# Performance work log

Hardware: AMD Instinct MI355X
Metric: run time of the kernel (lower is better)

## Reference

```python
import jax, jax.numpy as jnp
import numpy as np

DIM = 384
EPS = 1e-12  # F.normalize default eps


def setup_inputs() -> dict:
    key = jax.random.key(0)
    ks = jax.random.split(key, 6)
    b, c, h, w = 4, DIM, 64, 64
    x = jax.random.normal(ks[0], (b, c, h, w), dtype=jnp.float32)
    gamma = jnp.ones((c,), dtype=jnp.float32)  # WanRMS_norm gamma, init ones
    # 1x1 convs are per-pixel linear maps: [out_c, in_c] weight + bias
    w_qkv = jax.random.normal(ks[1], (3 * c, c), dtype=jnp.float32) * (1.0 / np.sqrt(c))
    b_qkv = jax.random.normal(ks[2], (3 * c,), dtype=jnp.float32) * 0.01
    w_proj = jax.random.normal(ks[3], (c, c), dtype=jnp.float32) * (1.0 / np.sqrt(c))
    b_proj = jax.random.normal(ks[4], (c,), dtype=jnp.float32) * 0.01
    return {"x": x, "gamma": gamma, "w_qkv": w_qkv, "b_qkv": b_qkv,
            "w_proj": w_proj, "b_proj": b_proj}


def reference(x, gamma, w_qkv, b_qkv, w_proj, b_proj):
    b, c, h, w = x.shape
    identity = x
    # WanRMS_norm: F.normalize over channel dim * sqrt(dim) * gamma
    l2 = jnp.sqrt(jnp.sum(x * x, axis=1, keepdims=True))
    xn = x / jnp.maximum(l2, EPS) * jnp.sqrt(jnp.float32(c)) * gamma[None, :, None, None]
    # 1x1 conv qkv: [b, 3c, h, w]
    qkv = jnp.einsum("bchw,oc->bohw", xn, w_qkv) + b_qkv[None, :, None, None]
    # flatten spatial -> tokens: [b, 3c, s] -> q/k/v each [b, s, c]
    s = h * w
    qkv = qkv.reshape(b, 3 * c, s).transpose(0, 2, 1)  # [b, s, 3c]
    q, k, v = jnp.split(qkv, 3, axis=-1)
    # single-head scaled dot-product attention (non-causal, as in Wan SDPA call)
    scores = jnp.einsum("bqc,bkc->bqk", q, k) / jnp.sqrt(jnp.float32(c))
    attn = jax.nn.softmax(scores, axis=-1)
    out = jnp.einsum("bqk,bkc->bqc", attn, v)  # [b, s, c]
    out = out.transpose(0, 2, 1).reshape(b, c, h, w)
    # 1x1 proj conv + residual
    out = jnp.einsum("bchw,oc->bohw", out, w_proj) + b_proj[None, :, None, None]
    return out + identity
```

## Files before the change

kernel.cpp:

```cpp
#include <hip/hip_runtime.h>
#include <cstdint>
#include <cstddef>

typedef __bf16 bf16;
typedef __bf16 bf16x8 __attribute__((ext_vector_type(8)));
typedef float  f32x4 __attribute__((ext_vector_type(4)));
typedef float  f32x16 __attribute__((ext_vector_type(16)));
typedef int    i32x4 __attribute__((ext_vector_type(4)));
typedef int    i32x8 __attribute__((ext_vector_type(8)));

#define MFMA16(a, b, c) __builtin_amdgcn_mfma_f32_16x16x32_bf16((a), (b), (c), 0, 0, 0)
#define MFMA_MX(a, b, c) \
    __builtin_amdgcn_mfma_scale_f32_32x32x64_f8f6f4((a), (b), (c), 0, 0, 0, 0x7F, 0, 0x7F)

#if __has_builtin(__builtin_amdgcn_exp2f)
#define EXP2(x) __builtin_amdgcn_exp2f(x)
#else
#define EXP2(x) exp2f(x)
#endif

__device__ __forceinline__ uint8_t to_fp8(float v) {
    return (uint8_t)(__builtin_amdgcn_cvt_pk_fp8_f32(v, v, 0, false) & 0xff);
}

__device__ __forceinline__ i32x8 ld32(const void* p) {
    i32x4 a = *(const i32x4*)p;
    i32x4 b = *(const i32x4*)((const char*)p + 16);
    i32x8 r;
    r[0] = a[0]; r[1] = a[1]; r[2] = a[2]; r[3] = a[3];
    r[4] = b[0]; r[5] = b[1]; r[6] = b[2]; r[7] = b[3];
    return r;
}

__device__ __forceinline__ void gload16(const void* g, void* l) {
    __builtin_amdgcn_global_load_lds(
        (const __attribute__((address_space(1))) unsigned int*)g,
        (__attribute__((address_space(3))) unsigned int*)l,
        16, 0, 0);
}

__global__ __launch_bounds__(256) void norm_kernel(
    const float* __restrict__ x, const float* __restrict__ gamma,
    const float* __restrict__ wqkv, const float* __restrict__ wproj,
    bf16* __restrict__ xn, bf16* __restrict__ wq, bf16* __restrict__ wp)
{
    const int tid = threadIdx.x;
    const int blk = blockIdx.x;
    if (blk >= 256) {
        int t0 = (blk - 256) * 256 + tid;
        for (int t = t0; t < 1152 * 384 + 384 * 384; t += 128 * 256) {
            if (t < 1152 * 384) wq[t] = (bf16)wqkv[t];
            else                wp[t - 1152 * 384] = (bf16)wproj[t - 1152 * 384];
        }
        return;
    }
    __shared__ float sG[384];
    __shared__ float sS[4][64];
    __shared__ float sScale[64];
    __shared__ bf16  sT[64][392];
    const int w = tid >> 6, l = tid & 63;
    for (int i = tid; i < 384; i += 256) sG[i] = gamma[i];
    const int b = blk >> 6, p0 = (blk & 63) << 6;
    const float* xc = x + ((size_t)(b * 384 + 96 * w)) * 4096 + p0 + l;
    float v[96];
    float s0 = 0.f, s1 = 0.f;
#pragma unroll
    for (int c = 0; c < 96; c += 2) {
        v[c]     = xc[(size_t)c * 4096];
        v[c + 1] = xc[(size_t)(c + 1) * 4096];
        s0 += v[c] * v[c]; s1 += v[c + 1] * v[c + 1];
    }
    sS[w][l] = s0 + s1;
    __syncthreads();
    if (w == 0) {
        float t = (sS[0][l] + sS[1][l]) + (sS[2][l] + sS[3][l]);
        sScale[l] = 19.595917942265423f / fmaxf(sqrtf(t), 1e-12f);
    }
    __syncthreads();
    float sc = sScale[l];
#pragma unroll
    for (int c0 = 0; c0 < 96; c0 += 8) {
        bf16x8 v8;
#pragma unroll
        for (int j = 0; j < 8; ++j)
            v8[j] = (bf16)(v[c0 + j] * sc * sG[96 * w + c0 + j]);
        *(bf16x8*)(&sT[l][96 * w + c0]) = v8;
    }
    __syncthreads();
    const int r = tid >> 2, seg = tid & 3;
    const bf16* srow = &sT[r][seg * 96];
    bf16* drow = xn + (size_t)((b << 12) + p0 + r) * 384 + seg * 96;
#pragma unroll
    for (int j = 0; j < 12; ++j)
        *(i32x4*)(drow + j * 8) = *(const i32x4*)(srow + j * 8);
}

__device__ __forceinline__ void gemm_core_bt(
    bf16* sA, bf16* sB,
    const bf16* __restrict__ A, const bf16* __restrict__ B,
    const float* __restrict__ bias_m, const float* __restrict__ bias_n,
    uint8_t* __restrict__ Cout, const int mode, const int ldc,
    const int m0, const int n0)
{
    const int tid = threadIdx.x;
    const int l = tid & 63, w = tid >> 6;
    const int lo = l & 15, hi = l >> 4;
    const int wm = w >> 1, wn = w & 1;

    f32x4 acc[4][4] = {};

    for (int kt = 0; kt < 6; ++kt) {
        __syncthreads();
        const int k0 = kt * 64;
#pragma unroll
        for (int i = 0; i < 5; ++i) {
            int ci = i * 256 + tid;
            if (ci < 1152) {
                int row = ci / 9, off = ci % 9;
                gload16(A + (size_t)(m0 + row) * 384 + k0 + off * 8, (char*)sA + ci * 16);
                gload16(B + (size_t)(n0 + row) * 384 + k0 + off * 8, (char*)sB + ci * 16);
            }
        }
        __syncthreads();
#pragma unroll
        for (int ks = 0; ks < 2; ++ks) {
            bf16x8 af[4], bfr[4];
#pragma unroll
            for (int t = 0; t < 4; ++t)
                af[t] = *(const bf16x8*)(sA + (wm * 64 + t * 16 + lo) * 72 + ks * 32 + hi * 8);
#pragma unroll
            for (int t = 0; t < 4; ++t)
                bfr[t] = *(const bf16x8*)(sB + (wn * 64 + t * 16 + lo) * 72 + ks * 32 + hi * 8);
#pragma unroll
            for (int rt = 0; rt < 4; ++rt)
#pragma unroll
                for (int ct = 0; ct < 4; ++ct)
                    acc[rt][ct] = MFMA16(af[rt], bfr[ct], acc[rt][ct]);
        }
    }

#pragma unroll
    for (int rt = 0; rt < 4; ++rt) {
#pragma unroll
        for (int ct = 0; ct < 4; ++ct) {
            int mb = m0 + wm * 64 + rt * 16 + hi * 4;
            int n  = n0 + wn * 64 + ct * 16 + lo;
            if (mode == 0) {
                float bn = bias_n[n];
#pragma unroll
                for (int r = 0; r < 4; ++r)
                    Cout[(size_t)(mb + r) * ldc + n] = to_fp8(acc[rt][ct][r] + bn);
            } else {
#pragma unroll
                for (int r = 0; r < 4; ++r)
                    Cout[(size_t)(mb + r) * ldc + n] = to_fp8(acc[rt][ct][r] + bias_m[mb + r]);
            }
        }
    }
}

__global__ __launch_bounds__(256) void gemm_qkv(
    const bf16* __restrict__ xn, const bf16* __restrict__ wq,
    const float* __restrict__ b_qkv, uint8_t* __restrict__ qkb,
    uint8_t* __restrict__ vtb)
{
    __shared__ bf16 sA[128 * 72];
    __shared__ bf16 sB[128 * 72];
    const int id = blockIdx.x;
    if (id < 768) {
        const int xcd = id & 7, s = id >> 3;
        gemm_core_bt(sA, sB, xn, wq, nullptr, b_qkv, qkb, 0, 768,
                     (xcd * 16 + s / 6) * 128, (s % 6) * 128);
    } else {
        const int t = id - 768;
        const int xcd = t & 7, s = t >> 3;
        gemm_core_bt(sA, sB, wq + (size_t)768 * 384, xn, b_qkv + 768, nullptr,
                     vtb, 1, 16384, (s % 3) * 128, (xcd * 16 + s / 3) * 128);
    }
}

__global__ __launch_bounds__(256) void gemm_proj(
    const bf16* __restrict__ wp, const bf16* __restrict__ p0,
    const bf16* __restrict__ p1, const float* __restrict__ ml,
    const float* __restrict__ b_proj, const float* __restrict__ x,
    float* __restrict__ out)
{
    __shared__ bf16 sA[128 * 72];
    __shared__ bf16 sB[128 * 72];
    const int tid = threadIdx.x;
    const int l = tid & 63, w = tid >> 6;
    const int lo = l & 15, hi = l >> 4;
    const int wm = w >> 1, wn = w & 1;
    const int id = blockIdx.x;
    const int xcd = id & 7, s = id >> 3;
    const int m0 = (s % 3) * 128, n0 = (xcd * 16 + s / 3) * 128;

    f32x4 acc[4][4] = {};

    for (int kt = 0; kt < 6; ++kt) {
        __syncthreads();
        const int k0 = kt * 64;
#pragma unroll
        for (int i = 0; i < 5; ++i) {
            int ci = i * 256 + tid;
            if (ci < 1152) {
                int row = ci / 9, off = ci % 9;
                gload16(wp + (size_t)(m0 + row) * 384 + k0 + off * 8, (char*)sA + ci * 16);
                int tok = n0 + row;
                float2 ml0 = *(const float2*)(ml + (size_t)tok * 2);
                float2 ml1 = *(const float2*)(ml + (size_t)(16384 + tok) * 2);
                float mM = fmaxf(ml0.x, ml1.x);
                float a0 = EXP2(ml0.x - mM), a1 = EXP2(ml1.x - mM);
                float inv = 1.0f / (a0 * ml0.y + a1 * ml1.y);
                float w0 = a0 * inv, w1 = a1 * inv;
                size_t boff = (size_t)tok * 384 + k0 + off * 8;
                bf16x8 v0 = *(const bf16x8*)(p0 + boff);
                bf16x8 v1 = *(const bf16x8*)(p1 + boff);
                bf16x8 r;
#pragma unroll
                for (int j = 0; j < 8; ++j)
                    r[j] = (bf16)((float)v0[j] * w0 + (float)v1[j] * w1);
                *(bf16x8*)((char*)sB + ci * 16) = r;
            }
        }
        __syncthreads();
#pragma unroll
        for (int ks = 0; ks < 2; ++ks) {
            bf16x8 af[4], bfr[4];
#pragma unroll
            for (int t = 0; t < 4; ++t)
                af[t] = *(const bf16x8*)(sA + (wm * 64 + t * 16 + lo) * 72 + ks * 32 + hi * 8);
#pragma unroll
            for (int t = 0; t < 4; ++t)
                bfr[t] = *(const bf16x8*)(sB + (wn * 64 + t * 16 + lo) * 72 + ks * 32 + hi * 8);
#pragma unroll
            for (int rt = 0; rt < 4; ++rt)
#pragma unroll
                for (int ct = 0; ct < 4; ++ct)
                    acc[rt][ct] = MFMA16(af[rt], bfr[ct], acc[rt][ct]);
        }
    }

#pragma unroll
    for (int rt = 0; rt < 4; ++rt) {
#pragma unroll
        for (int ct = 0; ct < 4; ++ct) {
            int mb = m0 + wm * 64 + rt * 16 + hi * 4;
            int n  = n0 + wn * 64 + ct * 16 + lo;
            int bb = n >> 12, p = n & 4095;
#pragma unroll
            for (int r = 0; r < 4; ++r) {
                int m = mb + r;
                size_t idx = ((size_t)(bb * 384 + m)) * 4096 + p;
                out[idx] = acc[rt][ct][r] + b_proj[m] + x[idx];
            }
        }
    }
}

__global__ __launch_bounds__(256, 2) void flash_kernel(
    const uint8_t* __restrict__ qk, const uint8_t* __restrict__ vt,
    bf16* __restrict__ op0, bf16* __restrict__ op1, float* __restrict__ ml)
{
    extern __shared__ char smem[];
    uint8_t* sbase = (uint8_t*)smem;
    uint8_t* sV = sbase + 51200;
    const int tid = threadIdx.x;
    const int l = tid & 63, w = tid >> 6;
    const int l31 = l & 31, hi2 = l >> 5;
    const int wq = w >> 1, wd = w & 1;
    const int id = blockIdx.x;
    const int qt = id >> 3, bh = id & 7;
    const int b = bh >> 1, half = bh & 1;
    const int q0 = b * 4096 + (qt & 63) * 64;
    const int kvbase = b * 4096 + half * 2048;
    const int rev = (id >> 8) & 1;
    const int kvstart = kvbase + (rev ? 31 * 64 : 0);
    const int kstep = rev ? -49152 : 49152;
    const int vstep = rev ? -64 : 64;
    const float SC = 0.07362217057594547f;
    const float THR = 108.664f;

    uint32_t ksrc[7];
#pragma unroll
    for (int i = 0; i < 7; ++i) {
        int ci = i * 256 + tid;
        int row = ci / 25, off = ci % 25;
        ksrc[i] = (uint32_t)((kvstart + row) * 768 + 384 + off * 16);
    }
    uint32_t vsrc[8];
#pragma unroll
    for (int i = 0; i < 8; ++i) {
        int ci = i * 256 + tid;
        int row = ci / 5, off = ci % 5;
        vsrc[i] = (uint32_t)(row * 16384 + kvstart + off * 16);
    }
#pragma unroll
    for (int i = 0; i < 7; ++i) {
        if (i < 6 || tid < 64) gload16(qk + ksrc[i], sbase + i * 4096 + tid * 16);
        ksrc[i] += (uint32_t)kstep;
    }

    i32x8 qf[6];
    {
        const uint8_t* qrow = qk + (size_t)(q0 + wq * 32 + l31) * 768 + hi2 * 32;
#pragma unroll
        for (int ksw = 0; ksw < 6; ++ksw)
            qf[ksw] = ld32(qrow + ksw * 64);
    }

    f32x16 o[6] = {};
    float m = -1e30f, lsum = 0.f;

    __syncthreads();

    int c = 0;
    for (int kt = 0; kt < 32; ++kt) {
#pragma unroll
        for (int i = 0; i < 8; ++i) {
            if (i < 7 || tid < 128) gload16(vt + vsrc[i], sV + i * 4096 + tid * 16);
            vsrc[i] += (uint32_t)vstep;
        }
        if (kt < 31) {
            uint8_t* dst = sbase + (c ^ 1) * 25600;
#pragma unroll
            for (int i = 0; i < 7; ++i) {
                if (i < 6 || tid < 64) gload16(qk + ksrc[i], dst + i * 4096 + tid * 16);
                ksrc[i] += (uint32_t)kstep;
            }
        }

        const uint8_t* sK = sbase + c * 25600;
        f32x16 s0 = {}, s1 = {};
        __builtin_amdgcn_s_setprio(1);
#pragma unroll
        for (int ksw = 0; ksw < 6; ++ksw) {
            i32x8 ak0 = ld32(sK + (size_t)l31 * 400 + ksw * 64 + hi2 * 32);
            i32x8 ak1 = ld32(sK + (size_t)(32 + l31) * 400 + ksw * 64 + hi2 * 32);
            s0 = MFMA_MX(ak0, qf[ksw], s0);
            s1 = MFMA_MX(ak1, qf[ksw], s1);
        }
        __builtin_amdgcn_s_setprio(0);

        float a0 = fmaxf(fmaxf(s0[0],  s0[1]),  fmaxf(s0[2],  s0[3]));
        float a1 = fmaxf(fmaxf(s0[4],  s0[5]),  fmaxf(s0[6],  s0[7]));
        float a2 = fmaxf(fmaxf(s0[8],  s0[9]),  fmaxf(s0[10], s0[11]));
        float a3 = fmaxf(fmaxf(s0[12], s0[13]), fmaxf(s0[14], s0[15]));
        float b0 = fmaxf(fmaxf(s1[0],  s1[1]),  fmaxf(s1[2],  s1[3]));
        float b1 = fmaxf(fmaxf(s1[4],  s1[5]),  fmaxf(s1[6],  s1[7]));
        float b2 = fmaxf(fmaxf(s1[8],  s1[9]),  fmaxf(s1[10], s1[11]));
        float b3 = fmaxf(fmaxf(s1[12], s1[13]), fmaxf(s1[14], s1[15]));
        float mx = fmaxf(fmaxf(fmaxf(a0, a1), fmaxf(a2, a3)),
                         fmaxf(fmaxf(b0, b1), fmaxf(b2, b3)));
        mx = fmaxf(mx, __shfl_xor(mx, 32));
        if (__any(mx > m + THR)) {
            float mn = fmaxf(m, mx);
            float alpha = EXP2((m - mn) * SC);
            m = mn;
            lsum *= alpha;
#pragma unroll
            for (int dt = 0; dt < 6; ++dt)
#pragma unroll
                for (int r = 0; r < 16; ++r) o[dt][r] *= alpha;
        }
        float p0[16], p1[16];
        float msc = m * SC;
        float rsa = 0.f, rsb = 0.f, rsc = 0.f, rsd = 0.f;
#pragma unroll
        for (int r = 0; r < 16; r += 4) {
            p0[r]     = EXP2(fmaf(s0[r],     SC, -msc)); rsa += p0[r];
            p0[r + 1] = EXP2(fmaf(s0[r + 1], SC, -msc)); rsb += p0[r + 1];
            p0[r + 2] = EXP2(fmaf(s0[r + 2], SC, -msc)); rsc += p0[r + 2];
            p0[r + 3] = EXP2(fmaf(s0[r + 3], SC, -msc)); rsd += p0[r + 3];
        }
#pragma unroll
        for (int r = 0; r < 16; r += 4) {
            p1[r]     = EXP2(fmaf(s1[r],     SC, -msc)); rsa += p1[r];
            p1[r + 1] = EXP2(fmaf(s1[r + 1], SC, -msc)); rsb += p1[r + 1];
            p1[r + 2] = EXP2(fmaf(s1[r + 2], SC, -msc)); rsc += p1[r + 2];
            p1[r + 3] = EXP2(fmaf(s1[r + 3], SC, -msc)); rsd += p1[r + 3];
        }
        float rs = (rsa + rsb) + (rsc + rsd);
        rs += __shfl_xor(rs, 32);
        lsum += rs;

        int pk0[4], pk1[4];
#pragma unroll
        for (int i = 0; i < 4; ++i) {
            int d = __builtin_amdgcn_cvt_pk_fp8_f32(p0[4 * i], p0[4 * i + 1], 0, false);
            pk0[i] = __builtin_amdgcn_cvt_pk_fp8_f32(p0[4 * i + 2], p0[4 * i + 3], d, true);
            d = __builtin_amdgcn_cvt_pk_fp8_f32(p1[4 * i], p1[4 * i + 1], 0, false);
            pk1[i] = __builtin_amdgcn_cvt_pk_fp8_f32(p1[4 * i + 2], p1[4 * i + 3], d, true);
        }
        i32x8 pf;
#pragma unroll
        for (int i = 0; i < 4; ++i) {
            int x0 = __shfl_xor(pk0[i], 32);
            int x1 = __shfl_xor(pk1[i], 32);
            int own = hi2 ? pk1[i] : pk0[i];
            int oth = hi2 ? x1 : x0;
            pf[2 * i]     = hi2 ? oth : own;
            pf[2 * i + 1] = hi2 ? own : oth;
        }

        __syncthreads();

        __builtin_amdgcn_s_setprio(1);
#pragma unroll
        for (int dt = 0; dt < 6; ++dt) {
            i32x8 av = ld32(sV + (size_t)(wd * 192 + dt * 32 + l31) * 80 + hi2 * 32);
            o[dt] = MFMA_MX(av, pf, o[dt]);
        }
        __builtin_amdgcn_s_setprio(0);

        __syncthreads();
        c ^= 1;
    }

    float* tr = (float*)(smem + w * 4608);
    bf16* dst = half ? op1 : op0;
#pragma unroll
    for (int dt = 0; dt < 6; ++dt) {
#pragma unroll
        for (int r = 0; r < 16; ++r) {
            int d32 = (r & 3) + 8 * (r >> 2) + 4 * hi2;
            tr[l31 * 36 + d32] = o[dt][r];
        }
        f32x4 v0 = *(f32x4*)(tr + l31 * 36 + hi2 * 16 + 0);
        f32x4 v1 = *(f32x4*)(tr + l31 * 36 + hi2 * 16 + 4);
        f32x4 v2 = *(f32x4*)(tr + l31 * 36 + hi2 * 16 + 8);
        f32x4 v3 = *(f32x4*)(tr + l31 * 36 + hi2 * 16 + 12);
        bf16x8 h0, h1;
#pragma unroll
        for (int j = 0; j < 4; ++j) {
            h0[j] = (bf16)v0[j]; h0[4 + j] = (bf16)v1[j];
            h1[j] = (bf16)v2[j]; h1[4 + j] = (bf16)v3[j];
        }
        size_t tok = (size_t)(q0 + wq * 32 + l31);
        bf16* drow = dst + tok * 384 + wd * 192 + dt * 32 + hi2 * 16;
        *(bf16x8*)(drow + 0) = h0;
        *(bf16x8*)(drow + 8) = h1;
    }
    if (wd == 0 && hi2 == 0) {
        int tok = q0 + wq * 32 + l31;
        ml[(size_t)(half * 16384 + tok) * 2 + 0] = m * SC;
        ml[(size_t)(half * 16384 + tok) * 2 + 1] = lsum;
    }
}

extern "C" void kernel_launch(void* const* d_in, const int* in_sizes, int n_in,
                              void* d_out, int out_size, void* d_ws, size_t ws_size,
                              hipStream_t stream) {
    const float* x      = (const float*)d_in[0];
    const float* gamma  = (const float*)d_in[1];
    const float* w_qkv  = (const float*)d_in[2];
    const float* b_qkv  = (const float*)d_in[3];
    const float* w_proj = (const float*)d_in[4];
    const float* b_proj = (const float*)d_in[5];
    float* out = (float*)d_out;

    char* ws = (char*)d_ws;
    bf16* xn  = (bf16*)ws;    ws += (size_t)16384 * 384 * 2;
    uint8_t* qkb = (uint8_t*)ws; ws += (size_t)16384 * 768;
    uint8_t* vtb = (uint8_t*)ws; ws += (size_t)384 * 16384;
    bf16* ob  = (bf16*)ws;    ws += (size_t)16384 * 384 * 2;
    bf16* wqb = (bf16*)ws;    ws += (size_t)1152 * 384 * 2;
    bf16* wpb = (bf16*)ws;    ws += (size_t)384 * 384 * 2;
    float* mlb = (float*)ws;  ws += (size_t)2 * 16384 * 2 * 4;

    (void)hipFuncSetAttribute((const void*)flash_kernel,
                              hipFuncAttributeMaxDynamicSharedMemorySize, 81920);

    norm_kernel<<<384, 256, 0, stream>>>(x, gamma, w_qkv, w_proj, xn, wqb, wpb);
    gemm_qkv<<<1152, 256, 0, stream>>>(xn, wqb, b_qkv, qkb, vtb);
    flash_kernel<<<512, 256, 81920, stream>>>(qkb, vtb, xn, ob, mlb);
    gemm_proj<<<384, 256, 0, stream>>>(wpb, xn, ob, mlb, b_proj, x, out);
}
```

Measured before the change: 236.6 us.

## Stage GEMM epilogues through LDS for coalesced stores; drop reversed KV order

The fp8 QKV GEMM epilogue now writes the output tile into shared memory and then stores full 16-byte rows, instead of scattered byte stores. The projection GEMM epilogue stages fp32 accumulators through LDS in two passes, then does vectorized residual loads and stores with the bias added. The flash kernel drops the alternating reversed KV traversal that blocks with id bit 8 set used before. This costs extra barriers and LDS traffic, and removing the reversal may lose whatever L2 locality it was giving.

```diff
diff --git a/kernel.cpp b/kernel.cpp
--- a/kernel.cpp
+++ b/kernel.cpp
@@ -139,24 +139,34 @@
         }
     }
 
+    uint8_t* ctile = (uint8_t*)sA;
+    __syncthreads();
 #pragma unroll
     for (int rt = 0; rt < 4; ++rt) {
 #pragma unroll
         for (int ct = 0; ct < 4; ++ct) {
-            int mb = m0 + wm * 64 + rt * 16 + hi * 4;
-            int n  = n0 + wn * 64 + ct * 16 + lo;
+            int row_l = wm * 64 + rt * 16 + hi * 4;
+            int col_l = wn * 64 + ct * 16 + lo;
             if (mode == 0) {
-                float bn = bias_n[n];
+                float bn = bias_n[n0 + col_l];
 #pragma unroll
                 for (int r = 0; r < 4; ++r)
-                    Cout[(size_t)(mb + r) * ldc + n] = to_fp8(acc[rt][ct][r] + bn);
+                    ctile[(row_l + r) * 144 + col_l] = to_fp8(acc[rt][ct][r] + bn);
             } else {
 #pragma unroll
                 for (int r = 0; r < 4; ++r)
-                    Cout[(size_t)(mb + r) * ldc + n] = to_fp8(acc[rt][ct][r] + bias_m[mb + r]);
+                    ctile[(row_l + r) * 144 + col_l] =
+                        to_fp8(acc[rt][ct][r] + bias_m[m0 + row_l + r]);
             }
         }
     }
+    __syncthreads();
+    const int row = tid >> 1, hf = tid & 1;
+    const uint8_t* srow = ctile + row * 144 + hf * 64;
+    uint8_t* drow = Cout + (size_t)(m0 + row) * ldc + n0 + hf * 64;
+#pragma unroll
+    for (int j = 0; j < 4; ++j)
+        *(i32x4*)(drow + j * 16) = *(const i32x4*)(srow + j * 16);
 }
 
 __global__ __launch_bounds__(256) void gemm_qkv(
@@ -185,8 +195,9 @@
     const float* __restrict__ b_proj, const float* __restrict__ x,
     float* __restrict__ out)
 {
-    __shared__ bf16 sA[128 * 72];
-    __shared__ bf16 sB[128 * 72];
+    __shared__ char gsm[36864];
+    bf16* sA = (bf16*)gsm;
+    bf16* sB = (bf16*)(gsm + 18432);
     const int tid = threadIdx.x;
     const int l = tid & 63, w = tid >> 6;
     const int lo = l & 15, hi = l >> 4;
@@ -241,19 +252,35 @@
         }
     }
 
-#pragma unroll
-    for (int rt = 0; rt < 4; ++rt) {
-#pragma unroll
-        for (int ct = 0; ct < 4; ++ct) {
-            int mb = m0 + wm * 64 + rt * 16 + hi * 4;
-            int n  = n0 + wn * 64 + ct * 16 + lo;
-            int bb = n >> 12, p = n & 4095;
-#pragma unroll
-            for (int r = 0; r < 4; ++r) {
-                int m = mb + r;
-                size_t idx = ((size_t)(bb * 384 + m)) * 4096 + p;
-                out[idx] = acc[rt][ct][r] + b_proj[m] + x[idx];
-            }
+    float* tile = (float*)gsm;
+    const int bb = n0 >> 12, pp0 = n0 & 4095;
+    for (int pass = 0; pass < 2; ++pass) {
+        __syncthreads();
+        if (wm == pass) {
+#pragma unroll
+            for (int rt = 0; rt < 4; ++rt)
+#pragma unroll
+                for (int ct = 0; ct < 4; ++ct) {
+                    int row_l = rt * 16 + hi * 4;
+                    int col_l = wn * 64 + ct * 16 + lo;
+#pragma unroll
+                    for (int r = 0; r < 4; ++r)
+                        tile[(row_l + r) * 132 + col_l] = acc[rt][ct][r];
+                }
+        }
+        __syncthreads();
+        const int row = tid >> 2, qu = tid & 3;
+        const int mch = m0 + pass * 64 + row;
+        const float bp = b_proj[mch];
+        const size_t gbase = ((size_t)(bb * 384 + mch)) * 4096 + pp0 + qu * 32;
+        const float* trow = tile + row * 132 + qu * 32;
+#pragma unroll
+        for (int j = 0; j < 8; ++j) {
+            f32x4 a4 = *(const f32x4*)(trow + j * 4);
+            f32x4 x4 = *(const f32x4*)(x + gbase + j * 4);
+#pragma unroll
+            for (int k = 0; k < 4; ++k) a4[k] = a4[k] + bp + x4[k];
+            *(f32x4*)(out + gbase + j * 4) = a4;
         }
     }
 }
@@ -272,12 +299,8 @@
     const int id = blockIdx.x;
     const int qt = id >> 3, bh = id & 7;
     const int b = bh >> 1, half = bh & 1;
-    const int q0 = b * 4096 + (qt & 63) * 64;
+    const int q0 = b * 4096 + qt * 64;
     const int kvbase = b * 4096 + half * 2048;
-    const int rev = (id >> 8) & 1;
-    const int kvstart = kvbase + (rev ? 31 * 64 : 0);
-    const int kstep = rev ? -49152 : 49152;
-    const int vstep = rev ? -64 : 64;
     const float SC = 0.07362217057594547f;
     const float THR = 108.664f;
 
@@ -286,19 +309,19 @@
     for (int i = 0; i < 7; ++i) {
         int ci = i * 256 + tid;
         int row = ci / 25, off = ci % 25;
-        ksrc[i] = (uint32_t)((kvstart + row) * 768 + 384 + off * 16);
+        ksrc[i] = (uint32_t)((kvbase + row) * 768 + 384 + off * 16);
     }
     uint32_t vsrc[8];
 #pragma unroll
     for (int i = 0; i < 8; ++i) {
         int ci = i * 256 + tid;
         int row = ci / 5, off = ci % 5;
-        vsrc[i] = (uint32_t)(row * 16384 + kvstart + off * 16);
+        vsrc[i] = (uint32_t)(row * 16384 + kvbase + off * 16);
     }
 #pragma unroll
     for (int i = 0; i < 7; ++i) {
         if (i < 6 || tid < 64) gload16(qk + ksrc[i], sbase + i * 4096 + tid * 16);
-        ksrc[i] += (uint32_t)kstep;
+        ksrc[i] += 49152;
     }
 
     i32x8 qf[6];
@@ -319,14 +342,14 @@
 #pragma unroll
         for (int i = 0; i < 8; ++i) {
             if (i < 7 || tid < 128) gload16(vt + vsrc[i], sV + i * 4096 + tid * 16);
-            vsrc[i] += (uint32_t)vstep;
+            vsrc[i] += 64;
         }
         if (kt < 31) {
             uint8_t* dst = sbase + (c ^ 1) * 25600;
 #pragma unroll
             for (int i = 0; i < 7; ++i) {
                 if (i < 6 || tid < 64) gload16(qk + ksrc[i], dst + i * 4096 + tid * 16);
-                ksrc[i] += (uint32_t)kstep;
+                ksrc[i] += 49152;
             }
         }
 
```

Result: slower. 242.9 us (+2.7%).
